# Optimization experiments

Measured on AMD Instinct MI355X. Metric: run time of the kernel, lower is better.

## Reference

```python
import jax, jax.numpy as jnp
import numpy as np

EPS = 1e-12  # torch F.normalize eps

def _normalize(x):
    n = jnp.linalg.norm(x, axis=-1, keepdims=True)
    return x / jnp.maximum(n, EPS)

def setup_inputs() -> dict:
    key = jax.random.key(0)
    k1, k2, k3, k4 = jax.random.split(key, 4)
    bs, P = 32, 256
    V = P * P                      # 65536 vertices
    F = 2 * (P - 1) ** 2           # 130050 faces
    C = 6                          # triangles per vertex ring
    points = jax.random.normal(k1, (bs, 3, V), dtype=jnp.float32)
    faces = jax.random.randint(k2, (F, 3), 0, V, dtype=jnp.int32)
    vert_tri_indices = jax.random.randint(k3, (V, C), 0, F, dtype=jnp.int32)
    vert_tri_weights = jax.random.uniform(k4, (V, C, 1), dtype=jnp.float32)
    return {"points": points, "faces": faces,
            "vert_tri_indices": vert_tri_indices,
            "vert_tri_weights": vert_tri_weights}

def reference(points, faces, vert_tri_indices, vert_tri_weights):
    # points: [bs, 3, V] -> vrt: [bs, V, 3]
    vrt = jnp.transpose(points, (0, 2, 1))
    # face normals: gather the 3 vertices of each face, cross, normalize
    v0 = vrt[:, faces[:, 0]]                       # [bs, F, 3]
    v1 = vrt[:, faces[:, 1]] - v0
    v2 = vrt[:, faces[:, 2]] - v0
    face_normals = _normalize(jnp.cross(v1, v2))   # [bs, F, 3]
    # vertex normals: weighted sum over each vertex's triangle ring
    fn_group = face_normals[:, vert_tri_indices]   # [bs, V, C, 3]
    vertex_normals = (fn_group * vert_tri_weights).sum(axis=-2)  # [bs, V, 3]
    return _normalize(vertex_normals)
```

## Files before the change

kernel.cpp:

```cpp
#include <hip/hip_runtime.h>
#include <hip/hip_bf16.h>


#define XCDS 8
#define BPX  4

typedef float f32x4 __attribute__((ext_vector_type(4)));

__device__ __forceinline__ float mulf_pin(float a, float b) {
  float t = a * b;
  asm("" : "+v"(t));
  return t;
}

__device__ __forceinline__ float3 cross_lhs(float ax, float ay, float az,
                                            float bx, float by, float bz) {
  float cx = __builtin_fmaf(ay, bz, -mulf_pin(az, by));
  float cy = __builtin_fmaf(az, bx, -mulf_pin(ax, bz));
  float cz = __builtin_fmaf(ax, by, -mulf_pin(ay, bx));
  return make_float3(cx, cy, cz);
}

__device__ __forceinline__ void nt_store_f4(float4* p, float x, float y,
                                            float z, float w) {
  f32x4 r;
  r[0] = x; r[1] = y; r[2] = z; r[3] = w;
  __builtin_nontemporal_store(r, (f32x4*)p);
}

__global__ __launch_bounds__(256) void rend12_pack(
    const float* __restrict__ points,
    float4*      __restrict__ ptsI,
    int V) {
  int xcd = blockIdx.x % XCDS;
  int seq = blockIdx.x / XCDS;
  int v   = seq * 256 + threadIdx.x;
  size_t base = ((size_t)xcd * V + v) * BPX;
#pragma unroll
  for (int bl = 0; bl < BPX; ++bl) {
    int b = xcd * BPX + bl;
    const float* pb = points + (size_t)b * 3 * V;
    float x = __builtin_nontemporal_load(pb + v);
    float y = __builtin_nontemporal_load(pb + V + v);
    float z = __builtin_nontemporal_load(pb + 2 * V + v);
    ptsI[base + bl] = make_float4(x, y, z, 0.0f);
  }
}

__global__ __launch_bounds__(256) void rend12_face(
    const float4* __restrict__ ptsI,
    const int*    __restrict__ faces,
    float4*       __restrict__ fnI,
    int F, int V) {
  int xcd = blockIdx.x % XCDS;
  int g   = (blockIdx.x / XCDS) * 256 + threadIdx.x;
  int f   = g >> 2;
  int bl  = g & 3;
  if (f >= F) return;

  int i0 = __builtin_nontemporal_load(faces + 3 * f + 0);
  int i1 = __builtin_nontemporal_load(faces + 3 * f + 1);
  int i2 = __builtin_nontemporal_load(faces + 3 * f + 2);

  float4 p0 = ptsI[((size_t)xcd * V + i0) * BPX + bl];
  float4 p1 = ptsI[((size_t)xcd * V + i1) * BPX + bl];
  float4 p2 = ptsI[((size_t)xcd * V + i2) * BPX + bl];

  float ax = p1.x - p0.x, ay = p1.y - p0.y, az = p1.z - p0.z;
  float bx = p2.x - p0.x, by = p2.y - p0.y, bz = p2.z - p0.z;

  float3 c = cross_lhs(ax, ay, az, bx, by, bz);

  float n = sqrtf((c.x * c.x + c.y * c.y) + c.z * c.z);
  float d = fmaxf(n, 1e-12f);

  nt_store_f4(fnI + ((size_t)xcd * F + f) * BPX + bl,
              c.x / d, c.y / d, c.z / d, 0.0f);
}

__global__ __launch_bounds__(256) void rend12_vertex(
    const float4* __restrict__ fnI,
    const int*    __restrict__ vti,
    const float*  __restrict__ vtw,
    float*        __restrict__ out,
    int F, int V) {
  int xcd = blockIdx.x % XCDS;
  int g   = (blockIdx.x / XCDS) * 256 + threadIdx.x;
  int v   = g >> 2;
  int bl  = g & 3;
  if (v >= V) return;

  const int2*   t2 = (const int2*)(vti + (size_t)v * 6);
  const float2* w2 = (const float2*)(vtw + (size_t)v * 6);
  int2   t01 = t2[0], t23 = t2[1], t45 = t2[2];
  float2 w01 = w2[0], w23 = w2[1], w45 = w2[2];
  int   idx[6] = {t01.x, t01.y, t23.x, t23.y, t45.x, t45.y};
  float wgt[6] = {w01.x, w01.y, w23.x, w23.y, w45.x, w45.y};

  float sx = 0.f, sy = 0.f, sz = 0.f;
#pragma unroll
  for (int c = 0; c < 6; ++c) {
    float4 nr = fnI[((size_t)xcd * F + idx[c]) * BPX + bl];
    sx += nr.x * wgt[c];
    sy += nr.y * wgt[c];
    sz += nr.z * wgt[c];
  }

  float n = sqrtf((sx * sx + sy * sy) + sz * sz);
  float d = fmaxf(n, 1e-12f);

  int b = xcd * BPX + bl;
  size_t o = ((size_t)b * V + v) * 3;
  __builtin_nontemporal_store(sx / d, out + o + 0);
  __builtin_nontemporal_store(sy / d, out + o + 1);
  __builtin_nontemporal_store(sz / d, out + o + 2);
}

__global__ __launch_bounds__(256) void rend12_face_fb(
    const float* __restrict__ points,
    const int*   __restrict__ faces,
    float4*      __restrict__ fnorm,
    int F, int V) {
  int f = blockIdx.x * blockDim.x + threadIdx.x;
  int b = blockIdx.y;
  if (f >= F) return;

  int i0 = faces[3 * f + 0];
  int i1 = faces[3 * f + 1];
  int i2 = faces[3 * f + 2];

  const float* pb = points + (size_t)b * 3 * V;
  float ax = pb[i1] - pb[i0], ay = pb[V + i1] - pb[V + i0], az = pb[2 * V + i1] - pb[2 * V + i0];
  float bx = pb[i2] - pb[i0], by = pb[V + i2] - pb[V + i0], bz = pb[2 * V + i2] - pb[2 * V + i0];

  float3 c = cross_lhs(ax, ay, az, bx, by, bz);

  float n = sqrtf((c.x * c.x + c.y * c.y) + c.z * c.z);
  float d = fmaxf(n, 1e-12f);

  fnorm[(size_t)b * F + f] = make_float4(c.x / d, c.y / d, c.z / d, 0.0f);
}

__global__ __launch_bounds__(256) void rend12_vertex_fb(
    const float4* __restrict__ fnorm,
    const int*    __restrict__ vti,
    const float*  __restrict__ vtw,
    float*        __restrict__ out,
    int F, int V) {
  int v = blockIdx.x * blockDim.x + threadIdx.x;
  int b = blockIdx.y;
  if (v >= V) return;

  const float4* fb = fnorm + (size_t)b * F;
  float sx = 0.f, sy = 0.f, sz = 0.f;
#pragma unroll
  for (int c = 0; c < 6; ++c) {
    int    idx = vti[v * 6 + c];
    float  w   = vtw[v * 6 + c];
    float4 nr  = fb[idx];
    sx += nr.x * w;
    sy += nr.y * w;
    sz += nr.z * w;
  }
  float n = sqrtf((sx * sx + sy * sy) + sz * sz);
  float d = fmaxf(n, 1e-12f);
  size_t o = ((size_t)b * V + v) * 3;
  out[o + 0] = sx / d;
  out[o + 1] = sy / d;
  out[o + 2] = sz / d;
}

extern "C" void kernel_launch(void* const* d_in, const int* in_sizes, int n_in,
                              void* d_out, int out_size, void* d_ws, size_t ws_size,
                              hipStream_t stream) {
  const float* points = (const float*)d_in[0];
  const int*   faces  = (const int*)d_in[1];
  const int*   vti    = (const int*)d_in[2];
  const float* vtw    = (const float*)d_in[3];
  float*       out    = (float*)d_out;

  const int F  = in_sizes[1] / 3;
  const int V  = in_sizes[2] / 6;
  const int bs = (int)(in_sizes[0] / (3 * (size_t)V));

  const size_t ptsI_bytes = (size_t)bs * V * sizeof(float4);
  const size_t fnI_bytes  = (size_t)bs * F * sizeof(float4);

  const bool fast_ok = (ws_size >= ptsI_bytes + fnI_bytes) &&
                       (bs == XCDS * BPX) && (V % 256 == 0);

  if (fast_ok) {
    float4* ptsI = (float4*)d_ws;
    float4* fnI  = (float4*)((char*)d_ws + ptsI_bytes);
    const int vpb = V / 256;
    const int fqb = (F * BPX + 255) / 256;
    const int vqb = (V * BPX) / 256;

    rend12_pack<<<dim3(XCDS * vpb), dim3(256), 0, stream>>>(points, ptsI, V);
    rend12_face<<<dim3(XCDS * fqb), dim3(256), 0, stream>>>(ptsI, faces, fnI, F, V);
    rend12_vertex<<<dim3(XCDS * vqb), dim3(256), 0, stream>>>(fnI, vti, vtw, out, F, V);
  } else if (ws_size >= fnI_bytes) {
    float4* fnorm = (float4*)d_ws;
    rend12_face_fb<<<dim3((F + 255) / 256, bs), dim3(256), 0, stream>>>(
        points, faces, fnorm, F, V);
    rend12_vertex_fb<<<dim3((V + 255) / 256, bs), dim3(256), 0, stream>>>(
        fnorm, vti, vtw, out, F, V);
  }
}
```

Before: 178.2 us.

## Fuse face-normal computation into vertex kernel, recomputing ring face normals

Removes the separate face-normal kernel and its interleaved face-normal workspace. Each vertex thread gathers its six ring faces' vertex indices and points, and recomputes the normalized cross products inline before the weighted sum. This eliminates the write and random re-read of the large face-normal buffer and one launch, at the cost of recomputing each face normal several times and issuing more point gathers. The pack kernel is also restructured to one batch element per thread.

```diff
diff --git a/kernel.cpp b/kernel.cpp
--- a/kernel.cpp
+++ b/kernel.cpp
@@ -6,6 +6,8 @@
 #define BPX  4
 
 typedef float f32x4 __attribute__((ext_vector_type(4)));
+typedef float f32x2 __attribute__((ext_vector_type(2)));
+typedef int   i32x2 __attribute__((ext_vector_type(2)));
 
 __device__ __forceinline__ float mulf_pin(float a, float b) {
   float t = a * b;
@@ -21,65 +23,25 @@
   return make_float3(cx, cy, cz);
 }
 
-__device__ __forceinline__ void nt_store_f4(float4* p, float x, float y,
-                                            float z, float w) {
-  f32x4 r;
-  r[0] = x; r[1] = y; r[2] = z; r[3] = w;
-  __builtin_nontemporal_store(r, (f32x4*)p);
-}
-
-__global__ __launch_bounds__(256) void rend12_pack(
+__global__ __launch_bounds__(256) void rend15_pack(
     const float* __restrict__ points,
     float4*      __restrict__ ptsI,
     int V) {
   int xcd = blockIdx.x % XCDS;
-  int seq = blockIdx.x / XCDS;
-  int v   = seq * 256 + threadIdx.x;
-  size_t base = ((size_t)xcd * V + v) * BPX;
-#pragma unroll
-  for (int bl = 0; bl < BPX; ++bl) {
-    int b = xcd * BPX + bl;
-    const float* pb = points + (size_t)b * 3 * V;
-    float x = __builtin_nontemporal_load(pb + v);
-    float y = __builtin_nontemporal_load(pb + V + v);
-    float z = __builtin_nontemporal_load(pb + 2 * V + v);
-    ptsI[base + bl] = make_float4(x, y, z, 0.0f);
-  }
+  int g   = (blockIdx.x / XCDS) * 256 + threadIdx.x;
+  int v   = g >> 2;
+  int bl  = g & 3;
+  int b   = xcd * BPX + bl;
+  const float* pb = points + (size_t)b * 3 * V;
+  float x = __builtin_nontemporal_load(pb + v);
+  float y = __builtin_nontemporal_load(pb + V + v);
+  float z = __builtin_nontemporal_load(pb + 2 * V + v);
+  ptsI[((size_t)xcd * V + v) * BPX + bl] = make_float4(x, y, z, 0.0f);
 }
 
-__global__ __launch_bounds__(256) void rend12_face(
+__global__ __launch_bounds__(256) void rend15_fused(
     const float4* __restrict__ ptsI,
     const int*    __restrict__ faces,
-    float4*       __restrict__ fnI,
-    int F, int V) {
-  int xcd = blockIdx.x % XCDS;
-  int g   = (blockIdx.x / XCDS) * 256 + threadIdx.x;
-  int f   = g >> 2;
-  int bl  = g & 3;
-  if (f >= F) return;
-
-  int i0 = __builtin_nontemporal_load(faces + 3 * f + 0);
-  int i1 = __builtin_nontemporal_load(faces + 3 * f + 1);
-  int i2 = __builtin_nontemporal_load(faces + 3 * f + 2);
-
-  float4 p0 = ptsI[((size_t)xcd * V + i0) * BPX + bl];
-  float4 p1 = ptsI[((size_t)xcd * V + i1) * BPX + bl];
-  float4 p2 = ptsI[((size_t)xcd * V + i2) * BPX + bl];
-
-  float ax = p1.x - p0.x, ay = p1.y - p0.y, az = p1.z - p0.z;
-  float bx = p2.x - p0.x, by = p2.y - p0.y, bz = p2.z - p0.z;
-
-  float3 c = cross_lhs(ax, ay, az, bx, by, bz);
-
-  float n = sqrtf((c.x * c.x + c.y * c.y) + c.z * c.z);
-  float d = fmaxf(n, 1e-12f);
-
-  nt_store_f4(fnI + ((size_t)xcd * F + f) * BPX + bl,
-              c.x / d, c.y / d, c.z / d, 0.0f);
-}
-
-__global__ __launch_bounds__(256) void rend12_vertex(
-    const float4* __restrict__ fnI,
     const int*    __restrict__ vti,
     const float*  __restrict__ vtw,
     float*        __restrict__ out,
@@ -90,20 +52,45 @@
   int bl  = g & 3;
   if (v >= V) return;
 
-  const int2*   t2 = (const int2*)(vti + (size_t)v * 6);
-  const float2* w2 = (const float2*)(vtw + (size_t)v * 6);
-  int2   t01 = t2[0], t23 = t2[1], t45 = t2[2];
-  float2 w01 = w2[0], w23 = w2[1], w45 = w2[2];
-  int   idx[6] = {t01.x, t01.y, t23.x, t23.y, t45.x, t45.y};
-  float wgt[6] = {w01.x, w01.y, w23.x, w23.y, w45.x, w45.y};
+  i32x2 t0 = __builtin_nontemporal_load((const i32x2*)(vti + (size_t)v * 6) + 0);
+  i32x2 t1 = __builtin_nontemporal_load((const i32x2*)(vti + (size_t)v * 6) + 1);
+  i32x2 t2 = __builtin_nontemporal_load((const i32x2*)(vti + (size_t)v * 6) + 2);
+  f32x2 w0 = __builtin_nontemporal_load((const f32x2*)(vtw + (size_t)v * 6) + 0);
+  f32x2 w1 = __builtin_nontemporal_load((const f32x2*)(vtw + (size_t)v * 6) + 1);
+  f32x2 w2 = __builtin_nontemporal_load((const f32x2*)(vtw + (size_t)v * 6) + 2);
+
+  int   fi[6]  = {t0[0], t0[1], t1[0], t1[1], t2[0], t2[1]};
+  float wgt[6] = {w0[0], w0[1], w1[0], w1[1], w2[0], w2[1]};
+
+  int ia[6], ib[6], ic[6];
+#pragma unroll
+  for (int c = 0; c < 6; ++c) {
+    ia[c] = faces[3 * fi[c] + 0];
+    ib[c] = faces[3 * fi[c] + 1];
+    ic[c] = faces[3 * fi[c] + 2];
+  }
+
+  const float4* P = ptsI + (size_t)xcd * V * BPX;
+  float4 p0[6], p1[6], p2[6];
+#pragma unroll
+  for (int c = 0; c < 6; ++c) {
+    p0[c] = P[(size_t)ia[c] * BPX + bl];
+    p1[c] = P[(size_t)ib[c] * BPX + bl];
+    p2[c] = P[(size_t)ic[c] * BPX + bl];
+  }
 
   float sx = 0.f, sy = 0.f, sz = 0.f;
 #pragma unroll
   for (int c = 0; c < 6; ++c) {
-    float4 nr = fnI[((size_t)xcd * F + idx[c]) * BPX + bl];
-    sx += nr.x * wgt[c];
-    sy += nr.y * wgt[c];
-    sz += nr.z * wgt[c];
+    float ax = p1[c].x - p0[c].x, ay = p1[c].y - p0[c].y, az = p1[c].z - p0[c].z;
+    float bx = p2[c].x - p0[c].x, by = p2[c].y - p0[c].y, bz = p2[c].z - p0[c].z;
+    float3 cr = cross_lhs(ax, ay, az, bx, by, bz);
+    float n = sqrtf((cr.x * cr.x + cr.y * cr.y) + cr.z * cr.z);
+    float d = fmaxf(n, 1e-12f);
+    float fx = cr.x / d, fy = cr.y / d, fz = cr.z / d;
+    sx += fx * wgt[c];
+    sy += fy * wgt[c];
+    sz += fz * wgt[c];
   }
 
   float n = sqrtf((sx * sx + sy * sy) + sz * sz);
@@ -116,7 +103,7 @@
   __builtin_nontemporal_store(sz / d, out + o + 2);
 }
 
-__global__ __launch_bounds__(256) void rend12_face_fb(
+__global__ __launch_bounds__(256) void rend15_face_fb(
     const float* __restrict__ points,
     const int*   __restrict__ faces,
     float4*      __restrict__ fnorm,
@@ -141,7 +128,7 @@
   fnorm[(size_t)b * F + f] = make_float4(c.x / d, c.y / d, c.z / d, 0.0f);
 }
 
-__global__ __launch_bounds__(256) void rend12_vertex_fb(
+__global__ __launch_bounds__(256) void rend15_vertex_fb(
     const float4* __restrict__ fnorm,
     const int*    __restrict__ vti,
     const float*  __restrict__ vtw,
@@ -184,26 +171,23 @@
   const int bs = (int)(in_sizes[0] / (3 * (size_t)V));
 
   const size_t ptsI_bytes = (size_t)bs * V * sizeof(float4);
-  const size_t fnI_bytes  = (size_t)bs * F * sizeof(float4);
+  const size_t fn_bytes   = (size_t)bs * F * sizeof(float4);
 
-  const bool fast_ok = (ws_size >= ptsI_bytes + fnI_bytes) &&
-                       (bs == XCDS * BPX) && (V % 256 == 0);
+  const bool fast_ok = (ws_size >= ptsI_bytes) &&
+                       (bs == XCDS * BPX) && ((V * BPX) % 256 == 0);
 
   if (fast_ok) {
     float4* ptsI = (float4*)d_ws;
-    float4* fnI  = (float4*)((char*)d_ws + ptsI_bytes);
-    const int vpb = V / 256;
-    const int fqb = (F * BPX + 255) / 256;
-    const int vqb = (V * BPX) / 256;
+    const int qpb = (V * BPX) / 256;
 
-    rend12_pack<<<dim3(XCDS * vpb), dim3(256), 0, stream>>>(points, ptsI, V);
-    rend12_face<<<dim3(XCDS * fqb), dim3(256), 0, stream>>>(ptsI, faces, fnI, F, V);
-    rend12_vertex<<<dim3(XCDS * vqb), dim3(256), 0, stream>>>(fnI, vti, vtw, out, F, V);
-  } else if (ws_size >= fnI_bytes) {
+    rend15_pack <<<dim3(XCDS * qpb), dim3(256), 0, stream>>>(points, ptsI, V);
+    rend15_fused<<<dim3(XCDS * qpb), dim3(256), 0, stream>>>(
+        ptsI, faces, vti, vtw, out, F, V);
+  } else if (ws_size >= fn_bytes) {
     float4* fnorm = (float4*)d_ws;
-    rend12_face_fb<<<dim3((F + 255) / 256, bs), dim3(256), 0, stream>>>(
+    rend15_face_fb<<<dim3((F + 255) / 256, bs), dim3(256), 0, stream>>>(
         points, faces, fnorm, F, V);
-    rend12_vertex_fb<<<dim3((V + 255) / 256, bs), dim3(256), 0, stream>>>(
+    rend15_vertex_fb<<<dim3((V + 255) / 256, bs), dim3(256), 0, stream>>>(
         fnorm, vti, vtw, out, F, V);
   }
 }
```

New measurement: 176.7 us. Within noise of the previous version (-0.8%).
